# Kernel optimization log

Hardware: AMD Instinct MI355X
Metric: run time of the kernel (lower is better)

## Reference

```python
import jax, jax.numpy as jnp
import numpy as np

ALPHA = 0.2        # LeakyReLU negative slope (config['alpha'])
NEG_INF = -9e15    # mask value from the original code


def setup_inputs() -> dict:
    key = jax.random.key(0)
    k1, k2, k3, k4 = jax.random.split(key, 4)
    N, Fin, Fout = 8192, 512, 256
    inp = jax.random.normal(k1, (N, Fin), dtype=jnp.float32)
    adj = jax.random.randint(k2, (N, N), 0, 2, dtype=jnp.int32)
    # xavier_uniform with gain=1.414
    limW = 1.414 * np.sqrt(6.0 / (Fin + Fout))
    W = jax.random.uniform(k3, (Fin, Fout), dtype=jnp.float32, minval=-limW, maxval=limW)
    lima = 1.414 * np.sqrt(6.0 / (2 * Fout + 1))
    a = jax.random.uniform(k4, (2 * Fout, 1), dtype=jnp.float32, minval=-lima, maxval=lima)
    return {"input": inp, "adj": adj, "W": W, "a": a}


def reference(input, adj, W, a):
    # h: [N, F]
    h = input @ W
    Fout = W.shape[1]
    # The original builds a_input[i, j] = concat(h_i, h_j) and dots with a.
    # Equivalently: e_ij = leakyrelu(h_i . a[:F] + h_j . a[F:]), computed
    # without the O(N^2 * 2F) intermediate.
    s1 = h @ a[:Fout, 0]   # [N] contribution from node i
    s2 = h @ a[Fout:, 0]   # [N] contribution from node j
    e = s1[:, None] + s2[None, :]                     # [N, N]
    e = jnp.where(e > 0, e, ALPHA * e)                # LeakyReLU
    scores = jnp.where(adj > 0, e, NEG_INF)
    attention = jax.nn.softmax(scores, axis=1)        # row-wise softmax
    # dropout is identity in inference mode (training=False)
    h_prime = attention @ h                           # [N, F]
    return jax.nn.elu(h_prime)                        # concat=True path
```

## Files before the change

### kernel.cpp

```cpp
#include <hip/hip_runtime.h>
#include <stdint.h>
#include <stddef.h>


#define N_NODES 8192
#define FIN     512
#define FOUT    256
#define LRALPHA 0.2f
#define MI_SHIFT 16.0f

typedef float f32x4 __attribute__((ext_vector_type(4)));
typedef short s16x8 __attribute__((ext_vector_type(8)));
typedef unsigned short u16x4 __attribute__((ext_vector_type(4)));
typedef int   i32x4 __attribute__((ext_vector_type(4)));
typedef unsigned long long u64;

typedef const uint32_t __attribute__((address_space(1)))* gas1_u32;
typedef uint32_t __attribute__((address_space(3)))* las3_u32;

__device__ __forceinline__ short f2bf_rne(float f) {
  uint32_t u = __builtin_bit_cast(uint32_t, f);
  u += 0x7fffu + ((u >> 16) & 1u);
  return (short)(u >> 16);
}
__device__ __forceinline__ short f2bf_fast(float f) {
  uint32_t u = __builtin_bit_cast(uint32_t, f);
  return (short)((u + 0x8000u) >> 16);
}
__device__ __forceinline__ float bf2f(short s) {
  uint32_t u = ((uint32_t)(uint16_t)s) << 16;
  return __builtin_bit_cast(float, u);
}

__device__ __forceinline__ uint32_t lds_off(void* p) {
  return (uint32_t)(uintptr_t)(las3_u32)p;
}

__global__ __launch_bounds__(256) void k_prep(const float* __restrict__ W,
                                              uint16_t* __restrict__ WThi,
                                              uint16_t* __restrict__ WTlo) {
  const int idx = blockIdx.x * 256 + threadIdx.x;
  const int n = idx >> 9;
  const int k = idx & 511;
  float v = W[k * FOUT + n];
  short h = f2bf_rne(v);
  WThi[idx] = (uint16_t)h;
  WTlo[idx] = (uint16_t)f2bf_rne(v - bf2f(h));
}

__global__ __launch_bounds__(256, 4) void k_pre(const float* __restrict__ X,
                                                const uint16_t* __restrict__ WThi,
                                                const uint16_t* __restrict__ WTlo,
                                                const float* __restrict__ a,
                                                uint16_t* __restrict__ HTf,
                                                float* __restrict__ s1g,
                                                float* __restrict__ s2g) {
  __shared__ float ls1[16], ls2[16];
  __shared__ uint16_t tile[FOUT * 16];
  const int lane = threadIdx.x & 63;
  const int w    = threadIdx.x >> 6;

  const int m    = lane & 15;
  const int quad = lane >> 4;
  const int i0   = blockIdx.x * 16;
  const int colg = w * 64;

  f32x4 acc[4];
#pragma unroll
  for (int cb = 0; cb < 4; ++cb) { f32x4 z = {0.f,0.f,0.f,0.f}; acc[cb] = z; }

  for (int kt = 0; kt < FIN / 32; ++kt) {
    const int k0 = kt * 32 + quad * 8;
    const float* ap = X + (size_t)(i0 + m) * FIN + k0;
    f32x4 a0 = *(const f32x4*)ap;
    f32x4 a1 = *(const f32x4*)(ap + 4);
    s16x8 ahi, alo;
#pragma unroll
    for (int e = 0; e < 4; ++e) {
      short h0 = f2bf_rne(a0[e]); ahi[e] = h0; alo[e] = f2bf_rne(a0[e] - bf2f(h0));
      short h1 = f2bf_rne(a1[e]); ahi[4+e] = h1; alo[4+e] = f2bf_rne(a1[e] - bf2f(h1));
    }
#pragma unroll
    for (int cb = 0; cb < 4; ++cb) {
      const int n = colg + cb * 16 + m;
      s16x8 bhi = *(const s16x8*)(WThi + (size_t)n * FIN + k0);
      s16x8 blo = *(const s16x8*)(WTlo + (size_t)n * FIN + k0);
      acc[cb] = __builtin_amdgcn_mfma_f32_16x16x32_bf16(ahi, bhi, acc[cb], 0, 0, 0);
      acc[cb] = __builtin_amdgcn_mfma_f32_16x16x32_bf16(ahi, blo, acc[cb], 0, 0, 0);
      acc[cb] = __builtin_amdgcn_mfma_f32_16x16x32_bf16(alo, bhi, acc[cb], 0, 0, 0);
    }
  }

  float p1[4] = {0.f,0.f,0.f,0.f}, p2[4] = {0.f,0.f,0.f,0.f};
#pragma unroll
  for (int cb = 0; cb < 4; ++cb) {
    const int n = colg + cb * 16 + m;
    const float a1c = a[n];
    const float a2c = a[FOUT + n];
#pragma unroll
    for (int reg = 0; reg < 4; ++reg) {
      p1[reg] += acc[cb][reg] * a1c;
      p2[reg] += acc[cb][reg] * a2c;
    }
  }
#pragma unroll
  for (int off = 1; off <= 8; off <<= 1)
#pragma unroll
    for (int reg = 0; reg < 4; ++reg) {
      p1[reg] += __shfl_xor(p1[reg], off);
      p2[reg] += __shfl_xor(p2[reg], off);
    }
  if (threadIdx.x < 16) { ls1[threadIdx.x] = 0.f; ls2[threadIdx.x] = 0.f; }
  __syncthreads();
  if (m == 0) {
#pragma unroll
    for (int reg = 0; reg < 4; ++reg) {
      atomicAdd(&ls1[quad * 4 + reg], p1[reg]);
      atomicAdd(&ls2[quad * 4 + reg], p2[reg]);
    }
  }
#pragma unroll
  for (int cb = 0; cb < 4; ++cb) {
    const int col = colg + cb * 16 + m;
    u16x4 pk;
#pragma unroll
    for (int reg = 0; reg < 4; ++reg) pk[reg] = (uint16_t)f2bf_rne(acc[cb][reg]);
    *(u16x4*)(tile + col * 16 + quad * 4) = pk;
  }
  __syncthreads();
  const int t = threadIdx.x;
  if (t < 16) { s1g[i0 + t] = ls1[t]; s2g[i0 + t] = ls2[t]; }
  const int jt = i0 >> 5;
  const int qh = (i0 >> 4) & 1;
  const int c  = t >> 4;
  const int mm = t & 15;
#pragma unroll
  for (int qq = 0; qq < 2; ++qq) {
    uint4 v = *(const uint4*)(tile + (c * 16 + mm) * 16 + qq * 8);
    *(uint4*)(HTf + ((((size_t)jt * 16 + c) * 64) + (qh * 2 + qq) * 16 + mm) * 8) = v;
  }
}

__global__ __launch_bounds__(512, 4) void k_attn(const uint16_t* __restrict__ HTf,
                                                 const float* __restrict__ s1,
                                                 const float* __restrict__ s2,
                                                 const int* __restrict__ adj,
                                                 float* __restrict__ pout,
                                                 float* __restrict__ pden,
                                                 int split) {
  __shared__ uint16_t PL[2][2048];
  __shared__ uint16_t BL[2][8192];
  __shared__ int      AL[4][2048];
  __shared__ float lss2[1024];

  const int tid  = threadIdx.x;
  const int lane = tid & 63;
  const int w    = tid >> 6;
  const int m    = lane & 15;
  const int q    = lane >> 4;
  const int rg   = w >> 2, cg = w & 3;
  const int rr   = tid >> 3;
  const int cw   = tid & 7;
  const int i0   = blockIdx.x * 64;
  const int sp   = blockIdx.y;
  const int jrange = N_NODES / split;
  const int jbeg   = sp * jrange;
  const int jblk   = jbeg >> 5;
  const int nphase = jrange / 32;

  const float s1r = s1[i0 + rr];
  float mi = fmaxf(s1r + MI_SHIFT, LRALPHA * (s1r + MI_SHIFT));

  f32x4 acc[2][4];
#pragma unroll
  for (int rt = 0; rt < 2; ++rt)
#pragma unroll
    for (int cb = 0; cb < 4; ++cb) { f32x4 z = {0.f,0.f,0.f,0.f}; acc[rt][cb] = z; }
  float den = 0.f;

#define STAGE_B(pp, buf) do {                                                  \
    const uint16_t* s_ = HTf + (((size_t)(jblk + (pp))) << 13) + (w << 10) +   \
                         (lane << 3);                                          \
    __builtin_amdgcn_global_load_lds((gas1_u32)(const void*)s_,                \
        (las3_u32)(void*)(&BL[buf][w << 10]), 16, 0, 0);                       \
    __builtin_amdgcn_global_load_lds((gas1_u32)(const void*)(s_ + 512),        \
        (las3_u32)(void*)(&BL[buf][(w << 10) + 512]), 16, 0, 0);               \
  } while (0)

#define STAGE_A(pp, buf) do {                                                  \
    const int* s_ = adj + (size_t)(i0 + w * 8 + (lane >> 3)) * N_NODES +       \
                    jbeg + (pp) * 32 + (lane & 7) * 4;                         \
    __builtin_amdgcn_global_load_lds((gas1_u32)(const void*)s_,                \
        (las3_u32)(void*)(&AL[buf][(w << 8) + (lane << 2)]), 16, 0, 0);        \
  } while (0)

  STAGE_B(0, 0);
  STAGE_A(0, 0);
  STAGE_A(1, 1);
  STAGE_A(2, 2);

#pragma unroll 1
  for (int p = 0; p < nphase; ++p) {
    if ((p & 31) == 0) {
      __syncthreads();
      if (tid < 256) *(f32x4*)(lss2 + tid * 4) =
        *(const f32x4*)(s2 + jbeg + (p >> 5) * 1024 + tid * 4);
      __syncthreads();
    }
    const int pl = p & 31;
    const uint32_t aAL = lds_off(&AL[p & 3][rr * 32 + cw * 4]);
    const uint32_t aS2 = lds_off(&lss2[pl * 32 + cw * 4]);
    i32x4 A0; f32x4 sA;
    asm volatile("ds_read_b128 %0, %1" : "=v"(A0) : "v"(aAL) : "memory");
    asm volatile("ds_read_b128 %0, %1" : "=v"(sA) : "v"(aS2) : "memory");
    asm volatile("s_waitcnt lgkmcnt(0)" ::: "memory");
    __builtin_amdgcn_sched_barrier(0);
    u16x4 P0;
#pragma unroll
    for (int e = 0; e < 4; ++e) {
      float x0 = s1r + sA[e];
      float pv0 = __expf(fmaxf(x0, LRALPHA * x0) - mi);
      pv0 = A0[e] ? pv0 : 0.f;
      den += pv0; P0[e] = (uint16_t)f2bf_fast(pv0);
    }
    {
      const uint32_t aPL = lds_off(&PL[p & 1][((cw >> 1) * 64 + rr) * 8 + (cw & 3 & 1) * 4]);
      asm volatile("ds_write_b64 %0, %1" : : "v"(aPL), "v"(P0) : "memory");
    }
    if (p + 5 < nphase) {
      asm volatile("s_waitcnt vmcnt(1) lgkmcnt(0)" ::: "memory");
    } else {
      asm volatile("s_waitcnt vmcnt(0) lgkmcnt(0)" ::: "memory");
    }
    __builtin_amdgcn_s_barrier();
    __builtin_amdgcn_sched_barrier(0);
    if (p + 1 < nphase) STAGE_B(p + 1, (p + 1) & 1);
    if (p + 3 < nphase) STAGE_A(p + 3, (p + 3) & 3);
    const uint32_t aF = lds_off(&PL[p & 1][(q * 64 + rg * 32 + m) * 8]);
    const uint32_t aB = lds_off(&BL[p & 1][((cg * 4) << 9) + (lane << 3)]);
    s16x8 F0, F1, B0, B1, B2, B3;
    asm volatile("ds_read_b128 %0, %1"             : "=v"(F0) : "v"(aF) : "memory");
    asm volatile("ds_read_b128 %0, %1 offset:256"  : "=v"(F1) : "v"(aF) : "memory");
    asm volatile("ds_read_b128 %0, %1"             : "=v"(B0) : "v"(aB) : "memory");
    asm volatile("ds_read_b128 %0, %1 offset:1024" : "=v"(B1) : "v"(aB) : "memory");
    asm volatile("ds_read_b128 %0, %1 offset:2048" : "=v"(B2) : "v"(aB) : "memory");
    asm volatile("ds_read_b128 %0, %1 offset:3072" : "=v"(B3) : "v"(aB) : "memory");
    asm volatile("s_waitcnt lgkmcnt(0)" ::: "memory");
    __builtin_amdgcn_sched_barrier(0);
    __builtin_amdgcn_s_setprio(1);
    acc[0][0] = __builtin_amdgcn_mfma_f32_16x16x32_bf16(B0, F0, acc[0][0], 0, 0, 0);
    acc[1][0] = __builtin_amdgcn_mfma_f32_16x16x32_bf16(B0, F1, acc[1][0], 0, 0, 0);
    acc[0][1] = __builtin_amdgcn_mfma_f32_16x16x32_bf16(B1, F0, acc[0][1], 0, 0, 0);
    acc[1][1] = __builtin_amdgcn_mfma_f32_16x16x32_bf16(B1, F1, acc[1][1], 0, 0, 0);
    acc[0][2] = __builtin_amdgcn_mfma_f32_16x16x32_bf16(B2, F0, acc[0][2], 0, 0, 0);
    acc[1][2] = __builtin_amdgcn_mfma_f32_16x16x32_bf16(B2, F1, acc[1][2], 0, 0, 0);
    acc[0][3] = __builtin_amdgcn_mfma_f32_16x16x32_bf16(B3, F0, acc[0][3], 0, 0, 0);
    acc[1][3] = __builtin_amdgcn_mfma_f32_16x16x32_bf16(B3, F1, acc[1][3], 0, 0, 0);
    __builtin_amdgcn_s_setprio(0);
  }
#undef STAGE_B
#undef STAGE_A

  den += __shfl_xor(den, 1);
  den += __shfl_xor(den, 2);
  den += __shfl_xor(den, 4);
  if (cw == 0) pden[(size_t)sp * N_NODES + i0 + rr] = den;

#pragma unroll
  for (int rt = 0; rt < 2; ++rt)
#pragma unroll
    for (int cb = 0; cb < 4; ++cb) {
      const int row = i0 + rg * 32 + rt * 16 + m;
      const int col = cg * 64 + cb * 16 + q * 4;
      *(f32x4*)(pout + ((size_t)sp * N_NODES + row) * FOUT + col) = acc[rt][cb];
    }
}

__global__ __launch_bounds__(256) void k_reduce(const float* __restrict__ pout,
                                                const float* __restrict__ pden,
                                                float* __restrict__ out,
                                                int split) {
  const int gid = blockIdx.x * 256 + threadIdx.x;
  const int i = gid >> 6;
  const int c = (gid & 63) << 2;
  f32x4 sum = {0.f,0.f,0.f,0.f};
  float den = 0.f;
  for (int s = 0; s < split; ++s) {
    sum += *(const f32x4*)(pout + ((size_t)s * N_NODES + i) * FOUT + c);
    den += pden[(size_t)s * N_NODES + i];
  }
  const float inv = 1.0f / den;
  f32x4 r;
#pragma unroll
  for (int e = 0; e < 4; ++e) {
    float v = sum[e] * inv;
    r[e] = v > 0.f ? v : (__expf(v) - 1.0f);
  }
  *(f32x4*)(out + (size_t)i * FOUT + c) = r;
}

extern "C" void kernel_launch(void* const* d_in, const int* in_sizes, int n_in,
                              void* d_out, int out_size, void* d_ws, size_t ws_size,
                              hipStream_t stream) {
  const float* X   = (const float*)d_in[0];
  const int*   adj = (const int*)d_in[1];
  const float* W   = (const float*)d_in[2];
  const float* a   = (const float*)d_in[3];
  float* out = (float*)d_out;

  char* ws = (char*)d_ws;
  uint16_t* HTf  = (uint16_t*)ws;
  uint16_t* WThi = (uint16_t*)(ws + (4u << 20));
  uint16_t* WTlo = (uint16_t*)(ws + (4u << 20) + 262144);
  float*    s1   = (float*)(ws + (4u << 20) + 524288);
  float*    s2   = s1 + N_NODES;
  float*    pden = s2 + N_NODES;
  const size_t pout_off = (size_t)16u << 20;
  const size_t slab = (size_t)N_NODES * FOUT * sizeof(float);

  int split;
  if      (ws_size >= pout_off + 4 * slab) split = 4;
  else if (ws_size >= pout_off + 2 * slab) split = 2;
  else                                     split = 1;
  float* pout = (split == 1) ? out : (float*)(ws + pout_off);

  k_prep<<<dim3(512), dim3(256), 0, stream>>>(W, WThi, WTlo);
  k_pre<<<dim3(512), dim3(256), 0, stream>>>(X, WThi, WTlo, a, HTf, s1, s2);
  k_attn<<<dim3(N_NODES / 64, split), dim3(512), 0, stream>>>(HTf, s1, s2, adj, pout, pden, split);
  k_reduce<<<dim3(N_NODES * FOUT / 4 / 256), dim3(256), 0, stream>>>(pout, pden, out, split);
}
```

Measured before the change: 455.0 us.

## Compute attention probabilities directly in MFMA operand registers, drop LDS staging

Each wave now computes the softmax numerators straight into the MFMA A-operand layout, so the P tile no longer goes through LDS. Adjacency values are loaded from global memory into registers with a two-phase register prefetch instead of being staged into LDS. This removes the PL and AL shared buffers, one LDS write/read round trip and one barrier dependency per phase. The cost is that the exp work is repeated across the four column-group waves (each wave computes 32x32 probabilities), more registers are used for the prefetched adjacency, and each wave loads adjacency redundantly.

```diff
diff --git a/kernel.cpp b/kernel.cpp
--- a/kernel.cpp
+++ b/kernel.cpp
@@ -148,9 +148,7 @@
                                                  float* __restrict__ pout,
                                                  float* __restrict__ pden,
                                                  int split) {
-  __shared__ uint16_t PL[2][2048];
   __shared__ uint16_t BL[2][8192];
-  __shared__ int      AL[4][2048];
   __shared__ float lss2[1024];
 
   const int tid  = threadIdx.x;
@@ -159,8 +157,6 @@
   const int m    = lane & 15;
   const int q    = lane >> 4;
   const int rg   = w >> 2, cg = w & 3;
-  const int rr   = tid >> 3;
-  const int cw   = tid & 7;
   const int i0   = blockIdx.x * 64;
   const int sp   = blockIdx.y;
   const int jrange = N_NODES / split;
@@ -168,15 +164,21 @@
   const int jblk   = jbeg >> 5;
   const int nphase = jrange / 32;
 
-  const float s1r = s1[i0 + rr];
-  float mi = fmaxf(s1r + MI_SHIFT, LRALPHA * (s1r + MI_SHIFT));
+  const int row0 = rg * 32 + m;
+  const float s1r0 = s1[i0 + row0];
+  const float s1r1 = s1[i0 + row0 + 16];
+  const float mi0 = fmaxf(s1r0 + MI_SHIFT, LRALPHA * (s1r0 + MI_SHIFT));
+  const float mi1 = fmaxf(s1r1 + MI_SHIFT, LRALPHA * (s1r1 + MI_SHIFT));
 
   f32x4 acc[2][4];
 #pragma unroll
   for (int rt = 0; rt < 2; ++rt)
 #pragma unroll
     for (int cb = 0; cb < 4; ++cb) { f32x4 z = {0.f,0.f,0.f,0.f}; acc[rt][cb] = z; }
-  float den = 0.f;
+  float den0 = 0.f, den1 = 0.f;
+
+  const int* adjp0 = adj + (size_t)(i0 + row0) * N_NODES + jbeg + q * 8;
+  const int* adjp1 = adjp0 + (size_t)16 * N_NODES;
 
 #define STAGE_B(pp, buf) do {                                                  \
     const uint16_t* s_ = HTf + (((size_t)(jblk + (pp))) << 13) + (w << 10) +   \
@@ -187,17 +189,15 @@
         (las3_u32)(void*)(&BL[buf][(w << 10) + 512]), 16, 0, 0);               \
   } while (0)
 
-#define STAGE_A(pp, buf) do {                                                  \
-    const int* s_ = adj + (size_t)(i0 + w * 8 + (lane >> 3)) * N_NODES +       \
-                    jbeg + (pp) * 32 + (lane & 7) * 4;                         \
-    __builtin_amdgcn_global_load_lds((gas1_u32)(const void*)s_,                \
-        (las3_u32)(void*)(&AL[buf][(w << 8) + (lane << 2)]), 16, 0, 0);        \
-  } while (0)
-
   STAGE_B(0, 0);
-  STAGE_A(0, 0);
-  STAGE_A(1, 1);
-  STAGE_A(2, 2);
+  i32x4 A0a = *(const i32x4*)adjp0;
+  i32x4 A0b = *(const i32x4*)(adjp0 + 4);
+  i32x4 A0c = *(const i32x4*)adjp1;
+  i32x4 A0d = *(const i32x4*)(adjp1 + 4);
+  i32x4 A1a = *(const i32x4*)(adjp0 + 32);
+  i32x4 A1b = *(const i32x4*)(adjp0 + 36);
+  i32x4 A1c = *(const i32x4*)(adjp1 + 32);
+  i32x4 A1d = *(const i32x4*)(adjp1 + 36);
 
 #pragma unroll 1
   for (int p = 0; p < nphase; ++p) {
@@ -207,40 +207,51 @@
         *(const f32x4*)(s2 + jbeg + (p >> 5) * 1024 + tid * 4);
       __syncthreads();
     }
-    const int pl = p & 31;
-    const uint32_t aAL = lds_off(&AL[p & 3][rr * 32 + cw * 4]);
-    const uint32_t aS2 = lds_off(&lss2[pl * 32 + cw * 4]);
-    i32x4 A0; f32x4 sA;
-    asm volatile("ds_read_b128 %0, %1" : "=v"(A0) : "v"(aAL) : "memory");
-    asm volatile("ds_read_b128 %0, %1" : "=v"(sA) : "v"(aS2) : "memory");
-    asm volatile("s_waitcnt lgkmcnt(0)" ::: "memory");
-    __builtin_amdgcn_sched_barrier(0);
-    u16x4 P0;
-#pragma unroll
-    for (int e = 0; e < 4; ++e) {
-      float x0 = s1r + sA[e];
-      float pv0 = __expf(fmaxf(x0, LRALPHA * x0) - mi);
-      pv0 = A0[e] ? pv0 : 0.f;
-      den += pv0; P0[e] = (uint16_t)f2bf_fast(pv0);
-    }
-    {
-      const uint32_t aPL = lds_off(&PL[p & 1][((cw >> 1) * 64 + rr) * 8 + (cw & 3 & 1) * 4]);
-      asm volatile("ds_write_b64 %0, %1" : : "v"(aPL), "v"(P0) : "memory");
-    }
-    if (p + 5 < nphase) {
-      asm volatile("s_waitcnt vmcnt(1) lgkmcnt(0)" ::: "memory");
+    if (p + 2 < nphase) {
+      asm volatile("s_waitcnt vmcnt(4)" ::: "memory");
     } else {
-      asm volatile("s_waitcnt vmcnt(0) lgkmcnt(0)" ::: "memory");
+      asm volatile("s_waitcnt vmcnt(0)" ::: "memory");
     }
     __builtin_amdgcn_s_barrier();
     __builtin_amdgcn_sched_barrier(0);
     if (p + 1 < nphase) STAGE_B(p + 1, (p + 1) & 1);
-    if (p + 3 < nphase) STAGE_A(p + 3, (p + 3) & 3);
-    const uint32_t aF = lds_off(&PL[p & 1][(q * 64 + rg * 32 + m) * 8]);
-    const uint32_t aB = lds_off(&BL[p & 1][((cg * 4) << 9) + (lane << 3)]);
-    s16x8 F0, F1, B0, B1, B2, B3;
-    asm volatile("ds_read_b128 %0, %1"             : "=v"(F0) : "v"(aF) : "memory");
-    asm volatile("ds_read_b128 %0, %1 offset:256"  : "=v"(F1) : "v"(aF) : "memory");
+    i32x4 A2a = {0,0,0,0}, A2b = A2a, A2c = A2a, A2d = A2a;
+    if (p + 2 < nphase) {
+      const int* n0 = adjp0 + (size_t)(p + 2) * 32;
+      const int* n1 = adjp1 + (size_t)(p + 2) * 32;
+      A2a = *(const i32x4*)n0;
+      A2b = *(const i32x4*)(n0 + 4);
+      A2c = *(const i32x4*)n1;
+      A2d = *(const i32x4*)(n1 + 4);
+    }
+    const uint32_t aS2 = lds_off(&lss2[(p & 31) * 32 + q * 8]);
+    f32x4 sA, sB;
+    asm volatile("ds_read_b128 %0, %1"            : "=v"(sA) : "v"(aS2) : "memory");
+    asm volatile("ds_read_b128 %0, %1 offset:16"  : "=v"(sB) : "v"(aS2) : "memory");
+    asm volatile("s_waitcnt lgkmcnt(0)" ::: "memory");
+    __builtin_amdgcn_sched_barrier(0);
+    s16x8 F0, F1;
+#pragma unroll
+    for (int e = 0; e < 4; ++e) {
+      float x0 = s1r0 + sA[e];
+      float pv0 = __expf(fmaxf(x0, LRALPHA * x0) - mi0);
+      pv0 = A0a[e] ? pv0 : 0.f;
+      den0 += pv0; F0[e] = f2bf_fast(pv0);
+      float x1 = s1r0 + sB[e];
+      float pv1 = __expf(fmaxf(x1, LRALPHA * x1) - mi0);
+      pv1 = A0b[e] ? pv1 : 0.f;
+      den0 += pv1; F0[4 + e] = f2bf_fast(pv1);
+      float x2 = s1r1 + sA[e];
+      float pv2 = __expf(fmaxf(x2, LRALPHA * x2) - mi1);
+      pv2 = A0c[e] ? pv2 : 0.f;
+      den1 += pv2; F1[e] = f2bf_fast(pv2);
+      float x3 = s1r1 + sB[e];
+      float pv3 = __expf(fmaxf(x3, LRALPHA * x3) - mi1);
+      pv3 = A0d[e] ? pv3 : 0.f;
+      den1 += pv3; F1[4 + e] = f2bf_fast(pv3);
+    }
+    const uint32_t aB = lds_off(&BL[p & 1][(cg << 11) + (lane << 3)]);
+    s16x8 B0, B1, B2, B3;
     asm volatile("ds_read_b128 %0, %1"             : "=v"(B0) : "v"(aB) : "memory");
     asm volatile("ds_read_b128 %0, %1 offset:1024" : "=v"(B1) : "v"(aB) : "memory");
     asm volatile("ds_read_b128 %0, %1 offset:2048" : "=v"(B2) : "v"(aB) : "memory");
@@ -257,14 +268,17 @@
     acc[0][3] = __builtin_amdgcn_mfma_f32_16x16x32_bf16(B3, F0, acc[0][3], 0, 0, 0);
     acc[1][3] = __builtin_amdgcn_mfma_f32_16x16x32_bf16(B3, F1, acc[1][3], 0, 0, 0);
     __builtin_amdgcn_s_setprio(0);
+    A0a = A1a; A0b = A1b; A0c = A1c; A0d = A1d;
+    A1a = A2a; A1b = A2b; A1c = A2c; A1d = A2d;
   }
 #undef STAGE_B
-#undef STAGE_A
-
-  den += __shfl_xor(den, 1);
-  den += __shfl_xor(den, 2);
-  den += __shfl_xor(den, 4);
-  if (cw == 0) pden[(size_t)sp * N_NODES + i0 + rr] = den;
+
+  den0 += __shfl_xor(den0, 16); den0 += __shfl_xor(den0, 32);
+  den1 += __shfl_xor(den1, 16); den1 += __shfl_xor(den1, 32);
+  if (cg == 0 && lane < 16) {
+    pden[(size_t)sp * N_NODES + i0 + rg * 32 + lane]      = den0;
+    pden[(size_t)sp * N_NODES + i0 + rg * 32 + 16 + lane] = den1;
+  }
 
 #pragma unroll
   for (int rt = 0; rt < 2; ++rt)
```

Measured after the change: 489.8 us. +7.6%, slower.
